# Performance work log

Measured on AMD Instinct MI355X. Metric: run time of the kernel, lower is better.

Reference implementation:

```python
import jax, jax.numpy as jnp
import numpy as np

DIM = 128
KS = 7
HEADS = 4
HEAD_DIM = DIM // HEADS


def setup_inputs() -> dict:
    key = jax.random.key(0)
    ks = jax.random.split(key, 10)
    B, H, W, C = 4, 64, 64, DIM
    s = 0.02
    return {
        "x": jax.random.normal(ks[0], (B, H, W, C), jnp.float32),
        "qkv_w": jax.random.normal(ks[1], (C, 3 * C), jnp.float32) * s,
        "qkv_b": jnp.zeros((3 * C,), jnp.float32),
        "proj_w": jax.random.normal(ks[2], (C, C), jnp.float32) * s,
        "proj_b": jnp.zeros((C,), jnp.float32),
        "rpb": jax.random.normal(ks[3], (HEADS, 2 * KS - 1, 2 * KS - 1), jnp.float32) * s,
        "g1_w": jax.random.normal(ks[4], (C, C // 2), jnp.float32) * s,
        "g1_b": jnp.zeros((C // 2,), jnp.float32),
        "g2_w": jax.random.normal(ks[5], (C // 2, 1), jnp.float32) * s,
        "g2_b": jnp.zeros((1,), jnp.float32),
    }


def _neighborhood_attention(x, qkv_w, qkv_b, proj_w, proj_b, rpb):
    B, H, W, C = x.shape
    k = KS
    # qkv projection -> [B,H,W,3,heads,head_dim]
    qkv = (x @ qkv_w + qkv_b).reshape(B, H, W, 3, HEADS, HEAD_DIM)
    q = qkv[..., 0, :, :] * (HEAD_DIM ** -0.5)  # [B,H,W,h,d]
    kk = qkv[..., 1, :, :]
    v = qkv[..., 2, :, :]

    # Clamped sliding-window start indices (NATTEN semantics)
    sh = jnp.clip(jnp.arange(H) - k // 2, 0, H - k)  # [H]
    sw = jnp.clip(jnp.arange(W) - k // 2, 0, W - k)  # [W]
    idx_h = sh[:, None] + jnp.arange(k)[None, :]  # [H,k]
    idx_w = sw[:, None] + jnp.arange(k)[None, :]  # [W,k]

    # Gather neighborhood windows: [B,H,W,k,k,h,d]
    kwin = kk[:, idx_h[:, None, :, None], idx_w[None, :, None, :]]
    vwin = v[:, idx_h[:, None, :, None], idx_w[None, :, None, :]]

    # Relative position bias indices: (neighbor - query) + (k-1)
    bih = idx_h - jnp.arange(H)[:, None] + (k - 1)  # [H,k]
    biw = idx_w - jnp.arange(W)[:, None] + (k - 1)  # [W,k]
    # bias: [h,H,W,k,k] -> [H,W,h,k,k]
    bias = rpb[:, bih[:, None, :, None], biw[None, :, None, :]]
    bias = jnp.transpose(bias, (1, 2, 0, 3, 4))

    # scores: [B,H,W,h,k,k]
    scores = jnp.einsum('bxyhd,bxyklhd->bxyhkl', q, kwin) + bias[None]
    attn = jax.nn.softmax(scores.reshape(B, H, W, HEADS, k * k), axis=-1)
    attn = attn.reshape(B, H, W, HEADS, k, k)
    out = jnp.einsum('bxyhkl,bxyklhd->bxyhd', attn, vwin).reshape(B, H, W, C)
    return out @ proj_w + proj_b


def reference(x, qkv_w, qkv_b, proj_w, proj_b, rpb, g1_w, g1_b, g2_w, g2_b):
    attn_out = _neighborhood_attention(x, qkv_w, qkv_b, proj_w, proj_b, rpb)
    gate = jax.nn.sigmoid(jax.nn.relu(x @ g1_w + g1_b) @ g2_w + g2_b)  # [B,H,W,1]
    return attn_out * gate + x
```

## Files before the change

### kernel.cpp

```cpp
#include <hip/hip_runtime.h>
#include <math.h>

#define PIXELS 16384
#define C      128
#define KS     7
#define HEADS  4
#define HD     32
#define QSCALE 0.17677669529663687f

typedef __bf16 bf16x8 __attribute__((ext_vector_type(8)));
typedef __bf16 bf16x2 __attribute__((ext_vector_type(2)));
typedef float  f32x4  __attribute__((ext_vector_type(4)));
typedef float  f32x2  __attribute__((ext_vector_type(2)));

__device__ inline unsigned short f2bf(float f) {
    unsigned int u = __builtin_bit_cast(unsigned int, f);
    u += 0x7FFFu + ((u >> 16) & 1u);
    return (unsigned short)(u >> 16);
}
__device__ inline float bflo(unsigned int u) {
    return __builtin_bit_cast(float, u << 16);
}
__device__ inline float bfhi(unsigned int u) {
    return __builtin_bit_cast(float, u & 0xFFFF0000u);
}

__global__ __launch_bounds__(256) void prep_kernel(
    const float* __restrict__ qkv_w, const float* __restrict__ g1_w,
    const float* __restrict__ qkv_b, const float* __restrict__ g1_b,
    const float* __restrict__ proj_w,
    unsigned short* __restrict__ wT, unsigned short* __restrict__ pT,
    float* __restrict__ bias_ext)
{
    const int blk = blockIdx.x, tid = threadIdx.x;
    if (blk < 56) {
        int n = blk * 8 + (tid >> 5);
        int kq = tid & 31;
        float f0, f1, f2, f3;
        if (n < 384) {
            f0 = qkv_w[(kq*4+0)*384 + n]; f1 = qkv_w[(kq*4+1)*384 + n];
            f2 = qkv_w[(kq*4+2)*384 + n]; f3 = qkv_w[(kq*4+3)*384 + n];
        } else {
            int nn = n - 384;
            f0 = g1_w[(kq*4+0)*64 + nn]; f1 = g1_w[(kq*4+1)*64 + nn];
            f2 = g1_w[(kq*4+2)*64 + nn]; f3 = g1_w[(kq*4+3)*64 + nn];
        }
        ushort4 o; o.x = f2bf(f0); o.y = f2bf(f1); o.z = f2bf(f2); o.w = f2bf(f3);
        *(ushort4*)(wT + n*128 + kq*4) = o;
    } else if (blk < 72) {
        int n = (blk - 56) * 8 + (tid >> 5);
        int kq = tid & 31;
        ushort4 o;
        o.x = f2bf(proj_w[(kq*4+0)*128 + n]);
        o.y = f2bf(proj_w[(kq*4+1)*128 + n]);
        o.z = f2bf(proj_w[(kq*4+2)*128 + n]);
        o.w = f2bf(proj_w[(kq*4+3)*128 + n]);
        *(ushort4*)(pT + n*128 + kq*4) = o;
    } else {
        for (int idx = tid; idx < 448; idx += 256)
            bias_ext[idx] = (idx < 384) ? qkv_b[idx] : g1_b[idx - 384];
    }
}

__global__ __launch_bounds__(256) void gemm_qkvh_fused(
    const float* __restrict__ x, const unsigned short* __restrict__ wT,
    const float* __restrict__ bias_ext, const float* __restrict__ g2_w,
    const float* __restrict__ g2_b, unsigned short* __restrict__ qkvb,
    float* __restrict__ gate)
{
    __shared__ __align__(16) unsigned short As[64*128];
    __shared__ __align__(16) unsigned short Bs[64*128];
    __shared__ __align__(16) unsigned short Cs[64*64];
    const int grp = blockIdx.x;
    const int ntBeg = grp ? 4 : 0, ntEnd = grp ? 7 : 4;
    const int m0 = blockIdx.y * 64;
    const int tid = threadIdx.x;

#pragma unroll
    for (int it = 0; it < 4; it++) {
        int idx = tid + it*256, row = idx >> 4, c = idx & 15;
        const float* src = x + (size_t)(m0+row)*128 + c*8;
        float4 a = *(const float4*)src;
        float4 b2 = *(const float4*)(src + 4);
        uint4 v;
        v.x = (unsigned int)f2bf(a.x)  | ((unsigned int)f2bf(a.y)  << 16);
        v.y = (unsigned int)f2bf(a.z)  | ((unsigned int)f2bf(a.w)  << 16);
        v.z = (unsigned int)f2bf(b2.x) | ((unsigned int)f2bf(b2.y) << 16);
        v.w = (unsigned int)f2bf(b2.z) | ((unsigned int)f2bf(b2.w) << 16);
        *(uint4*)(As + row*128 + ((c ^ (row&7)) << 3)) = v;
    }

    const int wave = tid >> 6, lane = tid & 63;
    const int l15 = lane & 15, quad = lane >> 4;
    const int wm = (wave & 1) * 32, wn = (wave >> 1) * 32;

    for (int nt = ntBeg; nt < ntEnd; nt++) {
        const int n0 = nt * 64;
#pragma unroll
        for (int it = 0; it < 4; it++) {
            int idx = tid + it*256, row = idx >> 4, c = idx & 15;
            uint4 v = *(const uint4*)(wT + (size_t)(n0+row)*128 + c*8);
            *(uint4*)(Bs + row*128 + ((c ^ (row&7)) << 3)) = v;
        }
        __syncthreads();

        f32x4 acc[2][2] = {};
#pragma unroll
        for (int ks = 0; ks < 4; ks++) {
            bf16x8 af[2], bq[2];
#pragma unroll
            for (int mt = 0; mt < 2; mt++) {
                int m = wm + mt*16 + l15;
                af[mt] = *(const bf16x8*)(As + m*128 + (((ks*4+quad) ^ (m&7)) << 3));
            }
#pragma unroll
            for (int ntl = 0; ntl < 2; ntl++) {
                int n = wn + ntl*16 + l15;
                bq[ntl] = *(const bf16x8*)(Bs + n*128 + (((ks*4+quad) ^ (n&7)) << 3));
            }
#pragma unroll
            for (int mt = 0; mt < 2; mt++)
#pragma unroll
                for (int ntl = 0; ntl < 2; ntl++)
                    acc[mt][ntl] = __builtin_amdgcn_mfma_f32_16x16x32_bf16(
                        af[mt], bq[ntl], acc[mt][ntl], 0, 0, 0);
        }

        if (nt < 6) {
#pragma unroll
            for (int ntl = 0; ntl < 2; ntl++) {
                int nl = wn + ntl*16 + l15;
                int ng = n0 + nl;
                float qs = (ng < 128) ? QSCALE : 1.0f;
                float bv = bias_ext[ng];
#pragma unroll
                for (int mt = 0; mt < 2; mt++)
#pragma unroll
                    for (int r = 0; r < 4; r++) {
                        int ml = wm + mt*16 + quad*4 + r;
                        Cs[ml*64 + nl] = f2bf((acc[mt][ntl][r] + bv) * qs);
                    }
            }
            __syncthreads();
            int row = tid >> 2, part = tid & 3;
            uint4 a = *(const uint4*)(Cs + row*64 + part*16);
            uint4 b = *(const uint4*)(Cs + row*64 + part*16 + 8);
            unsigned short* dst = qkvb + (size_t)(m0+row)*384 + n0 + part*16;
            *(uint4*)dst = a;
            *(uint4*)(dst + 8) = b;
        } else {
            float* gpart = (float*)Cs;
            float rs[2][4];
#pragma unroll
            for (int mt = 0; mt < 2; mt++)
#pragma unroll
                for (int r = 0; r < 4; r++) rs[mt][r] = 0.0f;
#pragma unroll
            for (int ntl = 0; ntl < 2; ntl++) {
                int nl = wn + ntl*16 + l15;
                float bv = bias_ext[384 + nl];
                float gw = g2_w[nl];
#pragma unroll
                for (int mt = 0; mt < 2; mt++)
#pragma unroll
                    for (int r = 0; r < 4; r++) {
                        float h = acc[mt][ntl][r] + bv;
                        rs[mt][r] += fmaxf(h, 0.0f) * gw;
                    }
            }
#pragma unroll
            for (int off = 1; off <= 8; off <<= 1)
#pragma unroll
                for (int mt = 0; mt < 2; mt++)
#pragma unroll
                    for (int r = 0; r < 4; r++)
                        rs[mt][r] += __shfl_xor(rs[mt][r], off);
            if (l15 == 0) {
#pragma unroll
                for (int mt = 0; mt < 2; mt++)
#pragma unroll
                    for (int r = 0; r < 4; r++)
                        gpart[(wave >> 1)*64 + wm + mt*16 + quad*4 + r] = rs[mt][r];
            }
            __syncthreads();
            if (tid < 64) {
                float g = gpart[tid] + gpart[64 + tid] + g2_b[0];
                gate[m0 + tid] = 1.0f / (1.0f + __expf(-g));
            }
        }
    }
}

#define ATTN_PROJ_LDS (196*264*2 + 676*4 + 64*128*2 + 128*128*2)

__global__ __launch_bounds__(512) void attn_proj(
    const unsigned short* __restrict__ qkvb, const float* __restrict__ rpb,
    const unsigned short* __restrict__ pT, const float* __restrict__ proj_b,
    const float* __restrict__ gate, const float* __restrict__ x,
    float* __restrict__ out)
{
    extern __shared__ __align__(16) unsigned char dynsmem[];
    unsigned short* kvs = (unsigned short*)dynsmem;
    float* rpb_lds = (float*)(dynsmem + 196*264*2);
    unsigned short* As = (unsigned short*)(dynsmem + 196*264*2 + 676*4);
    unsigned short* Bs = (unsigned short*)(dynsmem + 196*264*2 + 676*4 + 64*128*2);
    float* Cs = (float*)dynsmem;

    const int bid = blockIdx.x;
    const int b = bid >> 6;
    const int tile = bid & 63;
    const int ti0 = (tile >> 3) * 8, tj0 = (tile & 7) * 8;
    int wr0 = ti0 - 3; wr0 = wr0 < 0 ? 0 : (wr0 > 50 ? 50 : wr0);
    int wc0 = tj0 - 3; wc0 = wc0 < 0 ? 0 : (wc0 > 50 ? 50 : wc0);

    const int tid = threadIdx.x;
    const int wave = tid >> 6, lane = tid & 63;
    const int h = wave & 3;
    const int pg = wave >> 2;
    const int half = lane >> 5;
    const int p5 = lane & 31;
    const int pi = pg * 4 + (p5 >> 3), pj = p5 & 7;
    const int i = ti0 + pi, j = tj0 + pj;
    int sh = i - 3; sh = sh < 0 ? 0 : (sh > 57 ? 57 : sh);
    int sw = j - 3; sw = sw < 0 ? 0 : (sw > 57 ? 57 : sw);
    const int dr = sh - wr0, dc = sw - wc0;
    const size_t gp = (size_t)(((b << 6) + i) << 6) + j;

    unsigned int qu[8];
    const unsigned short* qptr = qkvb + gp * 384 + h * 32 + half * 16;
    *(uint4*)(qu + 0) = *(const uint4*)(qptr + 0);
    *(uint4*)(qu + 4) = *(const uint4*)(qptr + 8);

    float rpb_v[2];
#pragma unroll
    for (int t = 0; t < 2; t++) {
        int idx = tid + t * 512;
        rpb_v[t] = (idx < 676) ? rpb[idx] : 0.0f;
    }

    for (int idx = tid; idx < 196 * 32; idx += 512) {
        int pos = idx >> 5, t = idx & 31;
        int wr = pos / 14, wc = pos - wr * 14;
        size_t gpos = (size_t)(((b << 6) + (wr0 + wr)) << 6) + (wc0 + wc);
        uint4 v = *(const uint4*)(qkvb + gpos * 384 + 128 + t * 8);
        *(uint4*)(kvs + pos * 264 + t * 8) = v;
    }

#pragma unroll
    for (int it = 0; it < 4; it++) {
        int idx = tid + it*512, row = idx >> 4, c = idx & 15;
        uint4 v = *(const uint4*)(pT + (size_t)row*128 + c*8);
        *(uint4*)(Bs + row*128 + ((c ^ (row&7)) << 3)) = v;
    }
#pragma unroll
    for (int t = 0; t < 2; t++) {
        int idx = tid + t * 512;
        if (idx < 676) rpb_lds[idx] = rpb_v[t];
    }
    __syncthreads();

    f32x2 acc2[8];
#pragma unroll
    for (int p = 0; p < 8; p++) acc2[p] = (f32x2){0.f, 0.f};
    float ssum = 0.0f;

    const float* rl = rpb_lds + h * 169;
    const int rbase = (sh - i + 6) * 13 + (sw - j + 6);
    const int hwbase = (dr * 14 + dc) * 264 + h * 32 + half * 16;

    for (int kr = 0; kr < 7; kr++) {
        const unsigned short* rowp = kvs + hwbase + kr * (14 * 264);
        const int ri = rbase + kr * 13;

        unsigned int ku[8], vu[8];
        *(uint4*)(ku + 0) = *(const uint4*)(rowp + 0);
        *(uint4*)(ku + 4) = *(const uint4*)(rowp + 8);
        *(uint4*)(vu + 0) = *(const uint4*)(rowp + 128);
        *(uint4*)(vu + 4) = *(const uint4*)(rowp + 136);

#pragma unroll
        for (int kc = 0; kc < 7; kc++) {
            unsigned int ku2[8], vu2[8];
            if (kc < 6) {
                const unsigned short* kpn = rowp + (kc + 1) * 264;
                *(uint4*)(ku2 + 0) = *(const uint4*)(kpn + 0);
                *(uint4*)(ku2 + 4) = *(const uint4*)(kpn + 8);
                *(uint4*)(vu2 + 0) = *(const uint4*)(kpn + 128);
                *(uint4*)(vu2 + 4) = *(const uint4*)(kpn + 136);
            }

            float s0 = 0.0f, s1 = 0.0f;
#if __has_builtin(__builtin_amdgcn_fdot2_f32_bf16)
#pragma unroll
            for (int p = 0; p < 4; p++) {
                s0 = __builtin_amdgcn_fdot2_f32_bf16(
                        __builtin_bit_cast(bf16x2, qu[p]),
                        __builtin_bit_cast(bf16x2, ku[p]), s0, false);
                s1 = __builtin_amdgcn_fdot2_f32_bf16(
                        __builtin_bit_cast(bf16x2, qu[p+4]),
                        __builtin_bit_cast(bf16x2, ku[p+4]), s1, false);
            }
#else
#pragma unroll
            for (int p = 0; p < 4; p++) {
                s0 += bflo(qu[p])   * bflo(ku[p])   + bfhi(qu[p])   * bfhi(ku[p]);
                s1 += bflo(qu[p+4]) * bflo(ku[p+4]) + bfhi(qu[p+4]) * bfhi(ku[p+4]);
            }
#endif
            float s = s0 + s1;
            s += __shfl_xor(s, 32);
            float e = __expf(s + rl[ri + kc]);
            ssum += e;

            f32x2 e2 = {e, e};
#pragma unroll
            for (int p = 0; p < 8; p++) {
                f32x2 v2 = {bflo(vu[p]), bfhi(vu[p])};
                acc2[p] += e2 * v2;
            }

            if (kc < 6) {
#pragma unroll
                for (int p = 0; p < 8; p++) { ku[p] = ku2[p]; vu[p] = vu2[p]; }
            }
        }
    }

    {
        const float inv = 1.0f / ssum;
        unsigned int o[8];
#pragma unroll
        for (int p = 0; p < 8; p++) {
            unsigned int lo = f2bf(acc2[p].x * inv);
            unsigned int hi = f2bf(acc2[p].y * inv);
            o[p] = lo | (hi << 16);
        }
        const int pix = pi * 8 + pj;
        const int c0 = h * 4 + half * 2;
        *(uint4*)(As + pix*128 + (((c0  ) ^ (pix&7)) << 3)) = *(const uint4*)(o + 0);
        *(uint4*)(As + pix*128 + (((c0+1) ^ (pix&7)) << 3)) = *(const uint4*)(o + 4);
    }
    __syncthreads();

    {
        const int l15 = lane & 15, quad = lane >> 4;
        const int wm = (wave & 1) * 32, wn = (wave >> 1) * 32;

        f32x4 acc[2][2] = {};
#pragma unroll
        for (int ks = 0; ks < 4; ks++) {
            bf16x8 af[2], bq[2];
#pragma unroll
            for (int mt = 0; mt < 2; mt++) {
                int m = wm + mt*16 + l15;
                af[mt] = *(const bf16x8*)(As + m*128 + (((ks*4+quad) ^ (m&7)) << 3));
            }
#pragma unroll
            for (int ntl = 0; ntl < 2; ntl++) {
                int n = wn + ntl*16 + l15;
                bq[ntl] = *(const bf16x8*)(Bs + n*128 + (((ks*4+quad) ^ (n&7)) << 3));
            }
#pragma unroll
            for (int mt = 0; mt < 2; mt++)
#pragma unroll
                for (int ntl = 0; ntl < 2; ntl++)
                    acc[mt][ntl] = __builtin_amdgcn_mfma_f32_16x16x32_bf16(
                        af[mt], bq[ntl], acc[mt][ntl], 0, 0, 0);
        }

#pragma unroll
        for (int ntl = 0; ntl < 2; ntl++) {
            int nl = wn + ntl*16 + l15;
            float bv = proj_b[nl];
#pragma unroll
            for (int mt = 0; mt < 2; mt++)
#pragma unroll
                for (int r = 0; r < 4; r++) {
                    int ml = wm + mt*16 + quad*4 + r;
                    Cs[ml*128 + nl] = acc[mt][ntl][r] + bv;
                }
        }
    }
    __syncthreads();

    {
        int pix = tid >> 3, part = tid & 7;
        int gi = ti0 + (pix >> 3), gj = tj0 + (pix & 7);
        size_t gr = (size_t)(((b << 6) + gi) << 6) + gj;
        float gv = gate[gr];
        const float* xr = x + gr*128 + part*16;
        float* orow = out + gr*128 + part*16;
#pragma unroll
        for (int q = 0; q < 4; q++) {
            float4 cv = *(const float4*)(Cs + pix*128 + part*16 + q*4);
            float4 xv = *(const float4*)(xr + q*4);
            float4 o;
            o.x = cv.x * gv + xv.x; o.y = cv.y * gv + xv.y;
            o.z = cv.z * gv + xv.z; o.w = cv.w * gv + xv.w;
            *(float4*)(orow + q*4) = o;
        }
    }
}

extern "C" void kernel_launch(void* const* d_in, const int* in_sizes, int n_in,
                              void* d_out, int out_size, void* d_ws, size_t ws_size,
                              hipStream_t stream)
{
    const float* x      = (const float*)d_in[0];
    const float* qkv_w  = (const float*)d_in[1];
    const float* qkv_b  = (const float*)d_in[2];
    const float* proj_w = (const float*)d_in[3];
    const float* proj_b = (const float*)d_in[4];
    const float* rpb    = (const float*)d_in[5];
    const float* g1_w   = (const float*)d_in[6];
    const float* g1_b   = (const float*)d_in[7];
    const float* g2_w   = (const float*)d_in[8];
    const float* g2_b   = (const float*)d_in[9];
    float* out = (float*)d_out;

    float* ws        = (float*)d_ws;
    float* gate      = ws;
    float* bias_ext  = gate + 16384;
    unsigned short* wT    = (unsigned short*)(bias_ext + 448);
    unsigned short* pT    = wT + 57344;
    unsigned short* qkvb  = pT + 16384;

    (void)in_sizes; (void)n_in; (void)out_size; (void)ws_size;

    static int lds_ok = -1;
    if (lds_ok < 0) {
        hipError_t ae = hipFuncSetAttribute(
            (const void*)attn_proj,
            hipFuncAttributeMaxDynamicSharedMemorySize, ATTN_PROJ_LDS);
        lds_ok = (ae == hipSuccess) ? 1 : 0;
    }

    prep_kernel<<<73, 256, 0, stream>>>(qkv_w, g1_w, qkv_b, g1_b, proj_w,
                                        wT, pT, bias_ext);
    gemm_qkvh_fused<<<dim3(2, 256), 256, 0, stream>>>(x, wT, bias_ext,
                                                      g2_w, g2_b, qkvb, gate);
    attn_proj<<<256, 512, ATTN_PROJ_LDS, stream>>>(qkvb, rpb, pT, proj_b,
                                                   gate, x, out);
}
```

Baseline: 110.2 us.

## Share K/V window loads between adjacent query pixels and pad LDS strides

Each lane group now handles two horizontally adjacent query pixels, splitting the head dimension across four lanes instead of two. Each lane walks an 8-wide column span so the K/V values loaded from LDS are reused for both pixels, with masking for the column offset between their windows. This roughly halves LDS reads per score. The qkv output staging buffer and the projection output buffer get padded row strides to reduce LDS bank conflicts. The cost is an extra shuffle reduction per score and some wasted exp/FMA work on masked columns. Reading bias at idx-1 relies on the rpb buffer being padded.

```diff
diff --git a/kernel.cpp b/kernel.cpp
--- a/kernel.cpp
+++ b/kernel.cpp
@@ -70,7 +70,7 @@
 {
     __shared__ __align__(16) unsigned short As[64*128];
     __shared__ __align__(16) unsigned short Bs[64*128];
-    __shared__ __align__(16) unsigned short Cs[64*64];
+    __shared__ __align__(16) unsigned short Cs[64*72];
     const int grp = blockIdx.x;
     const int ntBeg = grp ? 4 : 0, ntEnd = grp ? 7 : 4;
     const int m0 = blockIdx.y * 64;
@@ -138,13 +138,13 @@
 #pragma unroll
                     for (int r = 0; r < 4; r++) {
                         int ml = wm + mt*16 + quad*4 + r;
-                        Cs[ml*64 + nl] = f2bf((acc[mt][ntl][r] + bv) * qs);
+                        Cs[ml*72 + nl] = f2bf((acc[mt][ntl][r] + bv) * qs);
                     }
             }
             __syncthreads();
             int row = tid >> 2, part = tid & 3;
-            uint4 a = *(const uint4*)(Cs + row*64 + part*16);
-            uint4 b = *(const uint4*)(Cs + row*64 + part*16 + 8);
+            uint4 a = *(const uint4*)(Cs + row*72 + part*16);
+            uint4 b = *(const uint4*)(Cs + row*72 + part*16 + 8);
             unsigned short* dst = qkvb + (size_t)(m0+row)*384 + n0 + part*16;
             *(uint4*)dst = a;
             *(uint4*)(dst + 8) = b;
@@ -191,7 +191,7 @@
     }
 }
 
-#define ATTN_PROJ_LDS (196*264*2 + 676*4 + 64*128*2 + 128*128*2)
+#define ATTN_PROJ_LDS (196*264*2 + 684*4 + 64*128*2 + 128*128*2)
 
 __global__ __launch_bounds__(512) void attn_proj(
     const unsigned short* __restrict__ qkvb, const float* __restrict__ rpb,
@@ -202,8 +202,8 @@
     extern __shared__ __align__(16) unsigned char dynsmem[];
     unsigned short* kvs = (unsigned short*)dynsmem;
     float* rpb_lds = (float*)(dynsmem + 196*264*2);
-    unsigned short* As = (unsigned short*)(dynsmem + 196*264*2 + 676*4);
-    unsigned short* Bs = (unsigned short*)(dynsmem + 196*264*2 + 676*4 + 64*128*2);
+    unsigned short* As = (unsigned short*)(dynsmem + 196*264*2 + 684*4);
+    unsigned short* Bs = (unsigned short*)(dynsmem + 196*264*2 + 684*4 + 64*128*2);
     float* Cs = (float*)dynsmem;
 
     const int bid = blockIdx.x;
@@ -217,19 +217,22 @@
     const int wave = tid >> 6, lane = tid & 63;
     const int h = wave & 3;
     const int pg = wave >> 2;
-    const int half = lane >> 5;
-    const int p5 = lane & 31;
-    const int pi = pg * 4 + (p5 >> 3), pj = p5 & 7;
-    const int i = ti0 + pi, j = tj0 + pj;
-    int sh = i - 3; sh = sh < 0 ? 0 : (sh > 57 ? 57 : sh);
-    int sw = j - 3; sw = sw < 0 ? 0 : (sw > 57 ? 57 : sw);
-    const int dr = sh - wr0, dc = sw - wc0;
-    const size_t gp = (size_t)(((b << 6) + i) << 6) + j;
-
-    unsigned int qu[8];
-    const unsigned short* qptr = qkvb + gp * 384 + h * 32 + half * 16;
-    *(uint4*)(qu + 0) = *(const uint4*)(qptr + 0);
-    *(uint4*)(qu + 4) = *(const uint4*)(qptr + 8);
+    const int p4 = lane & 15;
+    const int qtr = lane >> 4;
+    const int pi = pg * 4 + (p4 >> 2);
+    const int a = p4 & 3;
+    const int i = ti0 + pi, j0 = tj0 + a * 2;
+    int sh  = i - 3;  sh  = sh  < 0 ? 0 : (sh  > 57 ? 57 : sh);
+    int sw0 = j0 - 3; sw0 = sw0 < 0 ? 0 : (sw0 > 57 ? 57 : sw0);
+    int sw1 = j0 - 2; sw1 = sw1 < 0 ? 0 : (sw1 > 57 ? 57 : sw1);
+    const int d01 = sw1 - sw0;
+    const int dr = sh - wr0, dcu = sw0 - wc0;
+    const size_t gp0 = (size_t)(((b << 6) + i) << 6) + j0;
+
+    unsigned int qa[4], qb[4];
+    const unsigned short* qp = qkvb + gp0 * 384 + h * 32 + qtr * 8;
+    *(uint4*)qa = *(const uint4*)qp;
+    *(uint4*)qb = *(const uint4*)(qp + 384);
 
     float rpb_v[2];
 #pragma unroll
@@ -255,38 +258,34 @@
 #pragma unroll
     for (int t = 0; t < 2; t++) {
         int idx = tid + t * 512;
-        if (idx < 676) rpb_lds[idx] = rpb_v[t];
+        if (idx < 684) rpb_lds[idx] = rpb_v[t];
     }
     __syncthreads();
 
-    f32x2 acc2[8];
-#pragma unroll
-    for (int p = 0; p < 8; p++) acc2[p] = (f32x2){0.f, 0.f};
-    float ssum = 0.0f;
+    f32x2 acc0[4], acc1[4];
+#pragma unroll
+    for (int p = 0; p < 4; p++) { acc0[p] = (f32x2){0.f,0.f}; acc1[p] = (f32x2){0.f,0.f}; }
+    float ssum0 = 0.0f, ssum1 = 0.0f;
 
     const float* rl = rpb_lds + h * 169;
-    const int rbase = (sh - i + 6) * 13 + (sw - j + 6);
-    const int hwbase = (dr * 14 + dc) * 264 + h * 32 + half * 16;
+    const int rb0 = (sh - i + 6) * 13 + (sw0 - j0 + 6);
 
     for (int kr = 0; kr < 7; kr++) {
-        const unsigned short* rowp = kvs + hwbase + kr * (14 * 264);
-        const int ri = rbase + kr * 13;
-
-        unsigned int ku[8], vu[8];
-        *(uint4*)(ku + 0) = *(const uint4*)(rowp + 0);
-        *(uint4*)(ku + 4) = *(const uint4*)(rowp + 8);
-        *(uint4*)(vu + 0) = *(const uint4*)(rowp + 128);
-        *(uint4*)(vu + 4) = *(const uint4*)(rowp + 136);
-
-#pragma unroll
-        for (int kc = 0; kc < 7; kc++) {
-            unsigned int ku2[8], vu2[8];
-            if (kc < 6) {
+        const unsigned short* rowp = kvs + ((dr + kr) * 14 + dcu) * 264
+                                         + h * 32 + qtr * 8;
+        const int ri = rb0 + kr * 13;
+
+        unsigned int ku[4], vu[4];
+        *(uint4*)ku = *(const uint4*)(rowp + 0);
+        *(uint4*)vu = *(const uint4*)(rowp + 128);
+
+#pragma unroll
+        for (int kc = 0; kc < 8; kc++) {
+            unsigned int ku2[4], vu2[4];
+            if (kc < 7) {
                 const unsigned short* kpn = rowp + (kc + 1) * 264;
-                *(uint4*)(ku2 + 0) = *(const uint4*)(kpn + 0);
-                *(uint4*)(ku2 + 4) = *(const uint4*)(kpn + 8);
-                *(uint4*)(vu2 + 0) = *(const uint4*)(kpn + 128);
-                *(uint4*)(vu2 + 4) = *(const uint4*)(kpn + 136);
+                *(uint4*)ku2 = *(const uint4*)(kpn + 0);
+                *(uint4*)vu2 = *(const uint4*)(kpn + 128);
             }
 
             float s0 = 0.0f, s1 = 0.0f;
@@ -294,51 +293,58 @@
 #pragma unroll
             for (int p = 0; p < 4; p++) {
                 s0 = __builtin_amdgcn_fdot2_f32_bf16(
-                        __builtin_bit_cast(bf16x2, qu[p]),
+                        __builtin_bit_cast(bf16x2, qa[p]),
                         __builtin_bit_cast(bf16x2, ku[p]), s0, false);
                 s1 = __builtin_amdgcn_fdot2_f32_bf16(
-                        __builtin_bit_cast(bf16x2, qu[p+4]),
-                        __builtin_bit_cast(bf16x2, ku[p+4]), s1, false);
+                        __builtin_bit_cast(bf16x2, qb[p]),
+                        __builtin_bit_cast(bf16x2, ku[p]), s1, false);
             }
 #else
 #pragma unroll
             for (int p = 0; p < 4; p++) {
-                s0 += bflo(qu[p])   * bflo(ku[p])   + bfhi(qu[p])   * bfhi(ku[p]);
-                s1 += bflo(qu[p+4]) * bflo(ku[p+4]) + bfhi(qu[p+4]) * bfhi(ku[p+4]);
+                s0 += bflo(qa[p]) * bflo(ku[p]) + bfhi(qa[p]) * bfhi(ku[p]);
+                s1 += bflo(qb[p]) * bflo(ku[p]) + bfhi(qb[p]) * bfhi(ku[p]);
             }
 #endif
-            float s = s0 + s1;
-            s += __shfl_xor(s, 32);
-            float e = __expf(s + rl[ri + kc]);
-            ssum += e;
-
-            f32x2 e2 = {e, e};
-#pragma unroll
-            for (int p = 0; p < 8; p++) {
+            s0 += __shfl_xor(s0, 16);  s0 += __shfl_xor(s0, 32);
+            s1 += __shfl_xor(s1, 16);  s1 += __shfl_xor(s1, 32);
+
+            const int idx = ri + kc;
+            float b1v = rl[idx - 1];
+            float b0v = rl[idx];
+            float e0 = (kc <= 6) ? __expf(s0 + b0v) : 0.0f;
+            float e1 = ((unsigned)(kc - d01) <= 6u) ? __expf(s1 + b1v) : 0.0f;
+            ssum0 += e0;  ssum1 += e1;
+
+            f32x2 e0v = {e0, e0}, e1v = {e1, e1};
+#pragma unroll
+            for (int p = 0; p < 4; p++) {
                 f32x2 v2 = {bflo(vu[p]), bfhi(vu[p])};
-                acc2[p] += e2 * v2;
-            }
-
-            if (kc < 6) {
-#pragma unroll
-                for (int p = 0; p < 8; p++) { ku[p] = ku2[p]; vu[p] = vu2[p]; }
+                acc0[p] += e0v * v2;
+                acc1[p] += e1v * v2;
+            }
+
+            if (kc < 7) {
+#pragma unroll
+                for (int p = 0; p < 4; p++) { ku[p] = ku2[p]; vu[p] = vu2[p]; }
             }
         }
     }
 
     {
-        const float inv = 1.0f / ssum;
-        unsigned int o[8];
-#pragma unroll
-        for (int p = 0; p < 8; p++) {
-            unsigned int lo = f2bf(acc2[p].x * inv);
-            unsigned int hi = f2bf(acc2[p].y * inv);
-            o[p] = lo | (hi << 16);
-        }
-        const int pix = pi * 8 + pj;
-        const int c0 = h * 4 + half * 2;
-        *(uint4*)(As + pix*128 + (((c0  ) ^ (pix&7)) << 3)) = *(const uint4*)(o + 0);
-        *(uint4*)(As + pix*128 + (((c0+1) ^ (pix&7)) << 3)) = *(const uint4*)(o + 4);
+        const float inv0 = 1.0f / ssum0, inv1 = 1.0f / ssum1;
+        unsigned int o0[4], o1[4];
+#pragma unroll
+        for (int p = 0; p < 4; p++) {
+            o0[p] = (unsigned int)f2bf(acc0[p].x * inv0)
+                  | ((unsigned int)f2bf(acc0[p].y * inv0) << 16);
+            o1[p] = (unsigned int)f2bf(acc1[p].x * inv1)
+                  | ((unsigned int)f2bf(acc1[p].y * inv1) << 16);
+        }
+        const int pix0 = pi * 8 + a * 2;
+        const int c = h * 4 + qtr;
+        *(uint4*)(As + pix0*128     + ((c ^ (pix0 & 7)) << 3))     = *(const uint4*)o0;
+        *(uint4*)(As + (pix0+1)*128 + ((c ^ ((pix0+1) & 7)) << 3)) = *(const uint4*)o1;
     }
     __syncthreads();
 
@@ -377,7 +383,7 @@
 #pragma unroll
                 for (int r = 0; r < 4; r++) {
                     int ml = wm + mt*16 + quad*4 + r;
-                    Cs[ml*128 + nl] = acc[mt][ntl][r] + bv;
+                    Cs[ml*132 + nl] = acc[mt][ntl][r] + bv;
                 }
         }
     }
@@ -392,7 +398,7 @@
         float* orow = out + gr*128 + part*16;
 #pragma unroll
         for (int q = 0; q < 4; q++) {
-            float4 cv = *(const float4*)(Cs + pix*128 + part*16 + q*4);
+            float4 cv = *(const float4*)(Cs + pix*132 + part*16 + q*4);
             float4 xv = *(const float4*)(xr + q*4);
             float4 o;
             o.x = cv.x * gv + xv.x; o.y = cv.y * gv + xv.y;
```

Measured after the change: 114.0 us. 1.03x slower.
